# Kernel optimization log

Hardware: AMD Instinct MI355X
Metric: run time of the kernel (lower is better)

The kernel has to match this reference:

```python
import jax, jax.numpy as jnp
import numpy as np

VOCAB, EMBED = 100000, 128
B, QLEN, DLEN = 1024, 32, 256
KERNEL_NUM, SIGMA, EXACT_SIGMA = 11, 0.1, 0.001
EPS = 1e-8  # torch F.cosine_similarity eps


def _kernel_mus(n):
    l_mu = [1.0]
    if n == 1:
        return l_mu
    bin_size = 2.0 / (n - 1)
    l_mu.append(1 - bin_size / 2)
    for i in range(1, n - 1):
        l_mu.append(round(l_mu[i] - bin_size, 5))
    return list(reversed(l_mu))


def _kernel_sigmas(n, sigma, exact_sigma):
    l_sigma = [exact_sigma]
    if n == 1:
        return l_sigma
    l_sigma += [sigma] * (n - 1)
    return list(reversed(l_sigma))


MUS = jnp.asarray(np.array(_kernel_mus(KERNEL_NUM), dtype=np.float32))      # [K]
SIGMAS = jnp.asarray(np.array(_kernel_sigmas(KERNEL_NUM, SIGMA, EXACT_SIGMA), dtype=np.float32))  # [K]


def setup_inputs() -> dict:
    key = jax.random.key(0)
    k = jax.random.split(key, 7)
    return {
        "emb": jax.random.normal(k[0], (VOCAB, EMBED), dtype=jnp.float32),
        "mlp_w": jax.random.normal(k[1], (1, KERNEL_NUM), dtype=jnp.float32) * 0.3,
        "mlp_b": jax.random.normal(k[2], (1,), dtype=jnp.float32) * 0.1,
        "query1": jax.random.randint(k[3], (B, QLEN), 0, VOCAB, dtype=jnp.int32).astype(jnp.int64),
        "doc1": jax.random.randint(k[4], (B, DLEN), 0, VOCAB, dtype=jnp.int32).astype(jnp.int64),
        "query2": jax.random.randint(k[5], (B, QLEN), 0, VOCAB, dtype=jnp.int32).astype(jnp.int64),
        "doc2": jax.random.randint(k[6], (B, DLEN), 0, VOCAB, dtype=jnp.int32).astype(jnp.int64),
    }


def _predict(emb, mlp_w, mlp_b, query, doc):
    qe = emb[query]                               # [B,Q,E]
    de = emb[doc]                                 # [B,D,E]
    qn = jnp.linalg.norm(qe, axis=-1)             # [B,Q]
    dn = jnp.linalg.norm(de, axis=-1)             # [B,D]
    dots = jnp.einsum("bqe,bde->bqd", qe, de)    # [B,Q,D]
    sim = dots / jnp.maximum(qn[:, :, None] * dn[:, None, :], EPS)
    # multi-Gaussian soft histogram: exp(-(sim-mu)^2/(2 sigma^2)), sum over doc,
    # log1p, sum over query  -> [B,K]
    z = (sim[..., None] - MUS) / SIGMAS           # [B,Q,D,K]
    K = jnp.exp(-0.5 * z * z)
    pooled = jnp.log1p(K.sum(axis=2)).sum(axis=1)  # [B,K]
    return pooled @ mlp_w.T + mlp_b               # [B,1]


def reference(emb, mlp_w, mlp_b, query1, doc1, query2, doc2):
    logits_1 = _predict(emb, mlp_w, mlp_b, query1, doc1)
    logits_2 = _predict(emb, mlp_w, mlp_b, query2, doc2)
    return jax.nn.sigmoid(logits_1 - logits_2)    # [B,1]
```

## Files before the change

### kernel.cpp

```cpp
#include <hip/hip_runtime.h>
#include <math.h>
#include <stdint.h>

#define VOCAB 100000
#define NB    1024
#define QLEN  32
#define DLEN  256
#define EMBED 128
#define KNUM  11

typedef __attribute__((ext_vector_type(8))) short bf16x8;
typedef __attribute__((ext_vector_type(4))) float f32x4;

#define HALF_L2E 0.7213475204444817f
#define TWO_L2E  2.8853900817779268f
#define EM4      0.018315638888734179f

#define SSTR  68
#define SHALF (16 * SSTR)

__global__ __launch_bounds__(256)
void cvt_table(const float* __restrict__ emb, ushort* __restrict__ ebf,
               float* __restrict__ inorm)
{
    const int row = blockIdx.x * 8 + (threadIdx.x >> 5);
    const int l32 = threadIdx.x & 31;
    const float4 v = *((const float4*)(emb + (size_t)row * EMBED) + l32);
    union { float f; unsigned u; } x0, x1, x2, x3;
    x0.f = v.x; x1.f = v.y; x2.f = v.z; x3.f = v.w;
    const unsigned r0 = x0.u + 0x8000u, r1 = x1.u + 0x8000u;
    const unsigned r2 = x2.u + 0x8000u, r3 = x3.u + 0x8000u;
    uint2 packed;
    packed.x = (r0 >> 16) | (r1 & 0xFFFF0000u);
    packed.y = (r2 >> 16) | (r3 & 0xFFFF0000u);
    *((uint2*)(ebf + (size_t)row * EMBED) + l32) = packed;
    x0.u = r0 & 0xFFFF0000u; x1.u = r1 & 0xFFFF0000u;
    x2.u = r2 & 0xFFFF0000u; x3.u = r3 & 0xFFFF0000u;
    float n = x0.f * x0.f + x1.f * x1.f + x2.f * x2.f + x3.f * x3.f;
    #pragma unroll
    for (int m = 1; m < 32; m <<= 1) n += __shfl_xor(n, m);
    if (l32 == 0) inorm[row] = __builtin_amdgcn_rsqf(n);
}

__device__ __forceinline__ void chain4(const f32x4 sv, float (&ksum)[KNUM])
{
    #pragma unroll
    for (int e = 0; e < 4; ++e) {
        const float s  = sv[e];
        const float z  = fmaf(s, 10.f, -1.f);
        const float e0 = exp2f(-HALF_L2E * (z * z));
        float ru = exp2f(fmaf(z,  TWO_L2E, -TWO_L2E));
        float rd = exp2f(fmaf(z, -TWO_L2E, -TWO_L2E));
        ksum[5] += e0;
        float tt = e0;
        tt *= ru; ksum[6] += tt; ru *= EM4;
        tt *= ru; ksum[7] += tt; ru *= EM4;
        tt *= ru; ksum[8] += tt; ru *= EM4;
        tt *= ru; ksum[9] += tt;
        tt = e0;
        tt *= rd; ksum[4] += tt; rd *= EM4;
        tt *= rd; ksum[3] += tt; rd *= EM4;
        tt *= rd; ksum[2] += tt; rd *= EM4;
        tt *= rd; ksum[1] += tt; rd *= EM4;
        tt *= rd; ksum[0] += tt;
        ksum[10] += (s > 0.995f) ? 1.f : 0.f;
    }
}

__device__ __forceinline__ void pool_half(float* __restrict__ wtile,
                                          const f32x4* __restrict__ a,
                                          const float* __restrict__ riq,
                                          const float* __restrict__ idn,
                                          float (*__restrict__ stot)[12],
                                          int mtbase, int l15, int quad)
{
    #pragma unroll
    for (int nt = 0; nt < 4; ++nt)
        #pragma unroll
        for (int r = 0; r < 4; ++r)
            wtile[(quad * 4 + r) * SSTR + nt * 16 + l15] = a[nt][r] * riq[r] * idn[nt];

    const float* rp = wtile + l15 * SSTR + quad * 16;
    float ksum[KNUM];
    #pragma unroll
    for (int k = 0; k < KNUM; ++k) ksum[k] = 0.f;
    #pragma unroll
    for (int i = 0; i < 4; ++i)
        chain4(*(const f32x4*)(rp + 4 * i), ksum);
    #pragma unroll
    for (int k = 0; k < KNUM; ++k) {
        ksum[k] += __shfl_xor(ksum[k], 16);
        ksum[k] += __shfl_xor(ksum[k], 32);
    }
    if (quad == 0) {
        #pragma unroll
        for (int k = 0; k < KNUM; ++k)
            atomicAdd(&stot[mtbase + l15][k], ksum[k]);
    }
}

__global__ __launch_bounds__(256, 2)
void knrm_pair6(const ushort* __restrict__ ebf,
                const float* __restrict__ inorm,
                const float* __restrict__ mlp_w,
                const int* __restrict__ q1, const int* __restrict__ d1,
                const int* __restrict__ q2, const int* __restrict__ d2,
                float* __restrict__ logits)
{
    const int b    = blockIdx.x;
    const int pair = blockIdx.y;
    const int t    = threadIdx.x;
    const int w    = t >> 6;
    const int l    = t & 63;
    const int l15  = l & 15;
    const int quad = l >> 4;

    const int* __restrict__ qry = (pair == 0 ? q1 : q2) + b * QLEN;
    const int* __restrict__ doc = (pair == 0 ? d1 : d2) + b * DLEN;

    __shared__ __align__(16) uint4 s_frag[16 * 256 + 2 * 256];
    __shared__ float s_dnorm[DLEN];
    __shared__ float s_qnorm[QLEN];
    __shared__ float s_tot[QLEN][12];

    #define TPOS(r, s) ((s) * 16 + (((r) + (s)) & 15))

    #pragma unroll
    for (int j = 0; j < 4; ++j)
        #pragma unroll
        for (int i = 0; i < 4; ++i) {
            const int r  = 4 * i + quad;
            const int id = doc[w * 64 + j * 16 + r];
            const uint4 v = *(const uint4*)(ebf + (size_t)id * EMBED + l15 * 8);
            s_frag[(w * 4 + j) * 256 + TPOS(r, l15)] = v;
        }
    {
        const int mt = w >> 1;
        #pragma unroll
        for (int i = 0; i < 2; ++i) {
            const int r  = (w & 1) * 8 + 4 * i + quad;
            const int id = qry[mt * 16 + r];
            const uint4 v = *(const uint4*)(ebf + (size_t)id * EMBED + l15 * 8);
            s_frag[4096 + mt * 256 + TPOS(r, l15)] = v;
        }
    }
    s_dnorm[w * 64 + l] = inorm[doc[w * 64 + l]];
    if (t < QLEN) s_qnorm[t] = inorm[qry[t]];
    #pragma unroll
    for (int i = t; i < QLEN * 12; i += 256) ((float*)s_tot)[i] = 0.f;

    __syncthreads();

    f32x4 acc[2][4];
    #pragma unroll
    for (int mt = 0; mt < 2; ++mt)
        #pragma unroll
        for (int j = 0; j < 4; ++j)
            acc[mt][j] = (f32x4){0.f, 0.f, 0.f, 0.f};
    #pragma unroll
    for (int kk = 0; kk < 4; ++kk) {
        const int s = quad + 4 * kk;
        const bf16x8 a0 = *(const bf16x8*)&s_frag[4096 +       TPOS(l15, s)];
        const bf16x8 a1 = *(const bf16x8*)&s_frag[4096 + 256 + TPOS(l15, s)];
        #pragma unroll
        for (int j = 0; j < 4; ++j) {
            const bf16x8 bb = *(const bf16x8*)&s_frag[(w * 4 + j) * 256 + TPOS(l15, s)];
            acc[0][j] = __builtin_amdgcn_mfma_f32_16x16x32_bf16(a0, bb, acc[0][j], 0, 0, 0);
            acc[1][j] = __builtin_amdgcn_mfma_f32_16x16x32_bf16(a1, bb, acc[1][j], 0, 0, 0);
        }
    }

    float idn[4];
    #pragma unroll
    for (int j = 0; j < 4; ++j) idn[j] = s_dnorm[w * 64 + j * 16 + l15];
    float riq[2][4];
    #pragma unroll
    for (int r = 0; r < 4; ++r) {
        riq[0][r] = s_qnorm[quad * 4 + r];
        riq[1][r] = s_qnorm[16 + quad * 4 + r];
    }

    asm volatile("s_waitcnt lgkmcnt(0)" ::: "memory");
    __builtin_amdgcn_sched_barrier(0);

    float* wtile = (float*)s_frag + w * 4096;
    pool_half(wtile, acc[0], riq[0], idn, s_tot, 0,  l15, quad);
    pool_half(wtile, acc[1], riq[1], idn, s_tot, 16, l15, quad);
    __syncthreads();

    if (t < QLEN) {
        float c = 0.f;
        #pragma unroll
        for (int k = 0; k < KNUM; ++k) c += mlp_w[k] * log1pf(s_tot[t][k]);
        #pragma unroll
        for (int mm = 1; mm < 32; mm <<= 1) c += __shfl_xor(c, mm);
        if (t == 0) logits[pair * NB + b] = c;
    }
    #undef TPOS
}

__device__ __forceinline__ bf16x8 cvt8(const float* p, float& nacc)
{
    uint4 a = *((const uint4*)p);
    uint4 b = *((const uint4*)(p + 4));
    unsigned u[8] = {a.x, a.y, a.z, a.w, b.x, b.y, b.z, b.w};
    bf16x8 r;
    #pragma unroll
    for (int i = 0; i < 8; ++i) {
        const unsigned q = u[i] + 0x8000u;
        r[i] = (short)(q >> 16);
        union { unsigned uu; float ff; } g; g.uu = q & 0xFFFF0000u;
        nacc = fmaf(g.ff, g.ff, nacc);
    }
    return r;
}

__global__ __launch_bounds__(256, 4)
void knrm_pair_fb(const float* __restrict__ emb,
                  const float* __restrict__ mlp_w,
                  const int* __restrict__ q1, const int* __restrict__ d1,
                  const int* __restrict__ q2, const int* __restrict__ d2,
                  float* __restrict__ logits)
{
    const int b    = blockIdx.x;
    const int pair = blockIdx.y;
    const int t    = threadIdx.x;
    const int w    = t >> 6;
    const int l15  = t & 15;
    const int quad = (t & 63) >> 4;

    const int* __restrict__ qry = (pair == 0 ? q1 : q2) + b * QLEN;
    const int* __restrict__ doc = (pair == 0 ? d1 : d2) + b * DLEN;

    __shared__ __align__(16) float s_sim[4 * SHALF];
    __shared__ float s_tot[QLEN][12];

    #pragma unroll
    for (int i = t; i < QLEN * 12; i += 256) ((float*)s_tot)[i] = 0.f;
    __syncthreads();

    const int qid0 = qry[l15], qid1 = qry[l15 + 16];
    int did[4];
    #pragma unroll
    for (int nt = 0; nt < 4; ++nt) did[nt] = doc[(w * 4 + nt) * 16 + l15];

    f32x4 acc[2][4];
    #pragma unroll
    for (int mt = 0; mt < 2; ++mt)
        #pragma unroll
        for (int nt = 0; nt < 4; ++nt)
            acc[mt][nt] = (f32x4){0.f, 0.f, 0.f, 0.f};

    float idn[4], riq[2][4];
    float* wtile = s_sim + w * SHALF;

    {
        float qn2[2] = {0.f, 0.f}, dn2[4] = {0.f, 0.f, 0.f, 0.f};
        const float* qp0 = emb + (size_t)qid0 * EMBED + quad * 8;
        const float* qp1 = emb + (size_t)qid1 * EMBED + quad * 8;
        #pragma unroll
        for (int kk = 0; kk < 4; ++kk) {
            const bf16x8 a0 = cvt8(qp0 + kk * 32, qn2[0]);
            const bf16x8 a1 = cvt8(qp1 + kk * 32, qn2[1]);
            #pragma unroll
            for (int nt = 0; nt < 4; ++nt) {
                const bf16x8 bb = cvt8(emb + (size_t)did[nt] * EMBED + quad * 8 + kk * 32, dn2[nt]);
                acc[0][nt] = __builtin_amdgcn_mfma_f32_16x16x32_bf16(a0, bb, acc[0][nt], 0, 0, 0);
                acc[1][nt] = __builtin_amdgcn_mfma_f32_16x16x32_bf16(a1, bb, acc[1][nt], 0, 0, 0);
            }
        }
        #pragma unroll
        for (int i = 0; i < 2; ++i) {
            qn2[i] += __shfl_xor(qn2[i], 16);
            qn2[i] += __shfl_xor(qn2[i], 32);
        }
        #pragma unroll
        for (int nt = 0; nt < 4; ++nt) {
            dn2[nt] += __shfl_xor(dn2[nt], 16);
            dn2[nt] += __shfl_xor(dn2[nt], 32);
            idn[nt] = __builtin_amdgcn_rsqf(dn2[nt]);
        }
        #pragma unroll
        for (int r = 0; r < 4; ++r) {
            riq[0][r] = __builtin_amdgcn_rsqf(__shfl(qn2[0], quad * 4 + r));
            riq[1][r] = __builtin_amdgcn_rsqf(__shfl(qn2[1], quad * 4 + r));
        }
    }

    pool_half(wtile, acc[0], riq[0], idn, s_tot, 0,  l15, quad);
    pool_half(wtile, acc[1], riq[1], idn, s_tot, 16, l15, quad);
    __syncthreads();

    if (t < QLEN) {
        float c = 0.f;
        #pragma unroll
        for (int k = 0; k < KNUM; ++k) c += mlp_w[k] * log1pf(s_tot[t][k]);
        #pragma unroll
        for (int mm = 1; mm < 32; mm <<= 1) c += __shfl_xor(c, mm);
        if (t == 0) logits[pair * NB + b] = c;
    }
}

__global__ __launch_bounds__(256)
void knrm_combine(const float* __restrict__ logits, float* __restrict__ out)
{
    const int i = blockIdx.x * blockDim.x + threadIdx.x;
    if (i < NB) {
        const float d = logits[i] - logits[NB + i];
        out[i] = 1.f / (1.f + __expf(-d));
    }
}

extern "C" void kernel_launch(void* const* d_in, const int* in_sizes, int n_in,
                              void* d_out, int out_size, void* d_ws, size_t ws_size,
                              hipStream_t stream)
{
    const float* emb   = (const float*)d_in[0];
    const float* mlp_w = (const float*)d_in[1];
    const int* q1 = (const int*)d_in[3];
    const int* d1 = (const int*)d_in[4];
    const int* q2 = (const int*)d_in[5];
    const int* d2 = (const int*)d_in[6];

    float* out = (float*)d_out;

    const size_t need = 2 * NB * 4
                      + (size_t)VOCAB * 4
                      + (size_t)VOCAB * EMBED * 2 + 256;
    if (ws_size >= need) {
        float*  logits = (float*)d_ws;
        float*  inorm  = logits + 2 * NB;
        ushort* ebf    = (ushort*)(inorm + VOCAB);
        cvt_table<<<VOCAB / 8, 256, 0, stream>>>(emb, ebf, inorm);
        knrm_pair6<<<dim3(NB, 2), 256, 0, stream>>>(ebf, inorm, mlp_w,
                                                    q1, d1, q2, d2, logits);
    } else {
        float* logits = (float*)d_ws;
        knrm_pair_fb<<<dim3(NB, 2), 256, 0, stream>>>(emb, mlp_w,
                                                      q1, d1, q2, d2, logits);
    }
    knrm_combine<<<(NB + 255) / 256, 256, 0, stream>>>((float*)d_ws, out);
}
```

Measured before the change: 155.9 us.

## Compute norms on the fly and stream doc tiles per wave to raise occupancy

The table-conversion kernel no longer computes inverse norms. The main kernel now derives query and doc norms from the bf16 fragments already loaded for the MFMA. Instead of staging all 256 doc rows in LDS, each wave streams four 16-row doc tiles through a small per-wave swizzled buffer, register-prefetching the next tile while the current one is consumed. This cuts LDS use so launch bounds can target 4 blocks per CU, and it removes the inorm table and gathers. The cost is extra per-tile waits and shuffle reductions, plus higher register pressure from the prefetch.

```diff
diff --git a/kernel.cpp b/kernel.cpp
--- a/kernel.cpp
+++ b/kernel.cpp
@@ -20,8 +20,7 @@
 #define SHALF (16 * SSTR)
 
 __global__ __launch_bounds__(256)
-void cvt_table(const float* __restrict__ emb, ushort* __restrict__ ebf,
-               float* __restrict__ inorm)
+void cvt_table(const float* __restrict__ emb, ushort* __restrict__ ebf)
 {
     const int row = blockIdx.x * 8 + (threadIdx.x >> 5);
     const int l32 = threadIdx.x & 31;
@@ -34,12 +33,6 @@
     packed.x = (r0 >> 16) | (r1 & 0xFFFF0000u);
     packed.y = (r2 >> 16) | (r3 & 0xFFFF0000u);
     *((uint2*)(ebf + (size_t)row * EMBED) + l32) = packed;
-    x0.u = r0 & 0xFFFF0000u; x1.u = r1 & 0xFFFF0000u;
-    x2.u = r2 & 0xFFFF0000u; x3.u = r3 & 0xFFFF0000u;
-    float n = x0.f * x0.f + x1.f * x1.f + x2.f * x2.f + x3.f * x3.f;
-    #pragma unroll
-    for (int m = 1; m < 32; m <<= 1) n += __shfl_xor(n, m);
-    if (l32 == 0) inorm[row] = __builtin_amdgcn_rsqf(n);
 }
 
 __device__ __forceinline__ void chain4(const f32x4 sv, float (&ksum)[KNUM])
@@ -99,9 +92,19 @@
     }
 }
 
-__global__ __launch_bounds__(256, 2)
-void knrm_pair6(const ushort* __restrict__ ebf,
-                const float* __restrict__ inorm,
+__device__ __forceinline__ float sumsq8(const bf16x8 v, float acc)
+{
+    #pragma unroll
+    for (int e = 0; e < 8; ++e) {
+        union { unsigned u; float f; } g;
+        g.u = ((unsigned)(unsigned short)v[e]) << 16;
+        acc = fmaf(g.f, g.f, acc);
+    }
+    return acc;
+}
+
+__global__ __launch_bounds__(256, 4)
+void knrm_pair7(const ushort* __restrict__ ebf,
                 const float* __restrict__ mlp_w,
                 const int* __restrict__ q1, const int* __restrict__ d1,
                 const int* __restrict__ q2, const int* __restrict__ d2,
@@ -118,38 +121,43 @@
     const int* __restrict__ qry = (pair == 0 ? q1 : q2) + b * QLEN;
     const int* __restrict__ doc = (pair == 0 ? d1 : d2) + b * DLEN;
 
-    __shared__ __align__(16) uint4 s_frag[16 * 256 + 2 * 256];
-    __shared__ float s_dnorm[DLEN];
-    __shared__ float s_qnorm[QLEN];
+    __shared__ __align__(16) float s_buf[4][SHALF];
+    __shared__ __align__(16) uint4 s_q[2 * 256];
     __shared__ float s_tot[QLEN][12];
 
-    #define TPOS(r, s) ((s) * 16 + (((r) + (s)) & 15))
-
-    #pragma unroll
-    for (int j = 0; j < 4; ++j)
-        #pragma unroll
-        for (int i = 0; i < 4; ++i) {
-            const int r  = 4 * i + quad;
-            const int id = doc[w * 64 + j * 16 + r];
-            const uint4 v = *(const uint4*)(ebf + (size_t)id * EMBED + l15 * 8);
-            s_frag[(w * 4 + j) * 256 + TPOS(r, l15)] = v;
-        }
-    {
-        const int mt = w >> 1;
-        #pragma unroll
-        for (int i = 0; i < 2; ++i) {
-            const int r  = (w & 1) * 8 + 4 * i + quad;
-            const int id = qry[mt * 16 + r];
-            const uint4 v = *(const uint4*)(ebf + (size_t)id * EMBED + l15 * 8);
-            s_frag[4096 + mt * 256 + TPOS(r, l15)] = v;
-        }
-    }
-    s_dnorm[w * 64 + l] = inorm[doc[w * 64 + l]];
-    if (t < QLEN) s_qnorm[t] = inorm[qry[t]];
+    #define SWZ(r, s) (((r) << 4) | (((s) ^ (r)) & 15))
+
+    uint4* wbuf = (uint4*)&s_buf[w][0];
+
+    #pragma unroll
+    for (int i = 0; i < 2; ++i) {
+        const int row = w * 8 + i * 4 + quad;
+        const int id  = qry[row];
+        const uint4 v = *(const uint4*)(ebf + (size_t)id * EMBED + l15 * 8);
+        s_q[(row >> 4) * 256 + SWZ(row & 15, l15)] = v;
+    }
     #pragma unroll
     for (int i = t; i < QLEN * 12; i += 256) ((float*)s_tot)[i] = 0.f;
-
     __syncthreads();
+
+    bf16x8 a0[4], a1[4];
+    float qn0 = 0.f, qn1 = 0.f;
+    #pragma unroll
+    for (int kk = 0; kk < 4; ++kk) {
+        const int s = quad + 4 * kk;
+        a0[kk] = *(const bf16x8*)&s_q[      SWZ(l15, s)];
+        a1[kk] = *(const bf16x8*)&s_q[256 + SWZ(l15, s)];
+        qn0 = sumsq8(a0[kk], qn0);
+        qn1 = sumsq8(a1[kk], qn1);
+    }
+    qn0 += __shfl_xor(qn0, 16); qn0 += __shfl_xor(qn0, 32);
+    qn1 += __shfl_xor(qn1, 16); qn1 += __shfl_xor(qn1, 32);
+    float riq[2][4];
+    #pragma unroll
+    for (int r = 0; r < 4; ++r) {
+        riq[0][r] = __builtin_amdgcn_rsqf(__shfl(qn0, quad * 4 + r));
+        riq[1][r] = __builtin_amdgcn_rsqf(__shfl(qn1, quad * 4 + r));
+    }
 
     f32x4 acc[2][4];
     #pragma unroll
@@ -157,33 +165,49 @@
         #pragma unroll
         for (int j = 0; j < 4; ++j)
             acc[mt][j] = (f32x4){0.f, 0.f, 0.f, 0.f};
-    #pragma unroll
-    for (int kk = 0; kk < 4; ++kk) {
-        const int s = quad + 4 * kk;
-        const bf16x8 a0 = *(const bf16x8*)&s_frag[4096 +       TPOS(l15, s)];
-        const bf16x8 a1 = *(const bf16x8*)&s_frag[4096 + 256 + TPOS(l15, s)];
-        #pragma unroll
-        for (int j = 0; j < 4; ++j) {
-            const bf16x8 bb = *(const bf16x8*)&s_frag[(w * 4 + j) * 256 + TPOS(l15, s)];
-            acc[0][j] = __builtin_amdgcn_mfma_f32_16x16x32_bf16(a0, bb, acc[0][j], 0, 0, 0);
-            acc[1][j] = __builtin_amdgcn_mfma_f32_16x16x32_bf16(a1, bb, acc[1][j], 0, 0, 0);
-        }
-    }
-
     float idn[4];
-    #pragma unroll
-    for (int j = 0; j < 4; ++j) idn[j] = s_dnorm[w * 64 + j * 16 + l15];
-    float riq[2][4];
-    #pragma unroll
-    for (int r = 0; r < 4; ++r) {
-        riq[0][r] = s_qnorm[quad * 4 + r];
-        riq[1][r] = s_qnorm[16 + quad * 4 + r];
-    }
-
-    asm volatile("s_waitcnt lgkmcnt(0)" ::: "memory");
-    __builtin_amdgcn_sched_barrier(0);
-
-    float* wtile = (float*)s_frag + w * 4096;
+    uint4 pf[4];
+
+    #pragma unroll
+    for (int i = 0; i < 4; ++i) {
+        const int id = doc[w * 64 + 4 * i + quad];
+        pf[i] = *(const uint4*)(ebf + (size_t)id * EMBED + l15 * 8);
+    }
+
+    #pragma unroll
+    for (int j = 0; j < 4; ++j) {
+        #pragma unroll
+        for (int i = 0; i < 4; ++i)
+            wbuf[SWZ(4 * i + quad, l15)] = pf[i];
+        if (j < 3) {
+            #pragma unroll
+            for (int i = 0; i < 4; ++i) {
+                const int id = doc[w * 64 + (j + 1) * 16 + 4 * i + quad];
+                pf[i] = *(const uint4*)(ebf + (size_t)id * EMBED + l15 * 8);
+            }
+        }
+        asm volatile("s_waitcnt lgkmcnt(0)" ::: "memory");
+        __builtin_amdgcn_sched_barrier(0);
+
+        bf16x8 bb[4];
+        float dn = 0.f;
+        #pragma unroll
+        for (int kk = 0; kk < 4; ++kk) {
+            bb[kk] = *(const bf16x8*)&wbuf[SWZ(l15, quad + 4 * kk)];
+            dn = sumsq8(bb[kk], dn);
+        }
+        dn += __shfl_xor(dn, 16); dn += __shfl_xor(dn, 32);
+        idn[j] = __builtin_amdgcn_rsqf(dn);
+
+        #pragma unroll
+        for (int kk = 0; kk < 4; ++kk) {
+            acc[0][j] = __builtin_amdgcn_mfma_f32_16x16x32_bf16(a0[kk], bb[kk], acc[0][j], 0, 0, 0);
+            acc[1][j] = __builtin_amdgcn_mfma_f32_16x16x32_bf16(a1[kk], bb[kk], acc[1][j], 0, 0, 0);
+        }
+        __builtin_amdgcn_sched_barrier(0);
+    }
+
+    float* wtile = &s_buf[w][0];
     pool_half(wtile, acc[0], riq[0], idn, s_tot, 0,  l15, quad);
     pool_half(wtile, acc[1], riq[1], idn, s_tot, 16, l15, quad);
     __syncthreads();
@@ -196,7 +220,7 @@
         for (int mm = 1; mm < 32; mm <<= 1) c += __shfl_xor(c, mm);
         if (t == 0) logits[pair * NB + b] = c;
     }
-    #undef TPOS
+    #undef SWZ
 }
 
 __device__ __forceinline__ bf16x8 cvt8(const float* p, float& nacc)
@@ -325,14 +349,12 @@
     float* out = (float*)d_out;
 
     const size_t need = 2 * NB * 4
-                      + (size_t)VOCAB * 4
                       + (size_t)VOCAB * EMBED * 2 + 256;
     if (ws_size >= need) {
         float*  logits = (float*)d_ws;
-        float*  inorm  = logits + 2 * NB;
-        ushort* ebf    = (ushort*)(inorm + VOCAB);
-        cvt_table<<<VOCAB / 8, 256, 0, stream>>>(emb, ebf, inorm);
-        knrm_pair6<<<dim3(NB, 2), 256, 0, stream>>>(ebf, inorm, mlp_w,
+        ushort* ebf    = (ushort*)(logits + 2 * NB);
+        cvt_table<<<VOCAB / 8, 256, 0, stream>>>(emb, ebf);
+        knrm_pair7<<<dim3(NB, 2), 256, 0, stream>>>(ebf, mlp_w,
                                                     q1, d1, q2, d2, logits);
     } else {
         float* logits = (float*)d_ws;
```

Result: faster. 147.1 us (-5.6%).
